# Performance work log

Measured on AMD Instinct MI355X. Metric: run time of the kernel, lower is better.

Reference implementation:

```python
import math
import jax, jax.numpy as jnp
import numpy as np

EPS = 1e-5
NUM_HEADS = 8

def gelu(x):
    return jax.nn.gelu(x, approximate=False)  # keras 'gelu' is exact

def layernorm(x, g, b):
    m = jnp.mean(x, axis=-1, keepdims=True)
    v = jnp.var(x, axis=-1, keepdims=True)
    return (x - m) * jax.lax.rsqrt(v + EPS) * g + b

def setup_inputs() -> dict:
    key = jax.random.key(0)
    ks = jax.random.split(key, 12)
    B, S, N, D = 2, 1, 2048, 256
    E = 256  # dim_emb == dim_out
    s_in = 1.0 / np.sqrt(D).astype(np.float32)
    s_e = 1.0 / np.sqrt(E).astype(np.float32)
    s_h = 1.0 / np.sqrt(4 * E).astype(np.float32)
    return {
        "X": jax.random.normal(ks[0], (B, S, N, D), jnp.float32),
        "Wq": jax.random.normal(ks[1], (D, E), jnp.float32) * s_in,
        "Wk": jax.random.normal(ks[2], (D, E), jnp.float32) * s_in,
        "Wv": jax.random.normal(ks[3], (D, E), jnp.float32) * s_in,
        "Wm": jax.random.normal(ks[4], (E, E), jnp.float32) * s_e,
        "bm": jnp.zeros((E,), jnp.float32),
        "W1": jax.random.normal(ks[5], (E, 4 * E), jnp.float32) * s_e,
        "bf1": jnp.zeros((4 * E,), jnp.float32),
        "W2": jax.random.normal(ks[6], (4 * E, E), jnp.float32) * s_h,
        "bf2": jnp.zeros((E,), jnp.float32),
        "ln0_g": jnp.ones((D,), jnp.float32),
        "ln0_b": jnp.zeros((D,), jnp.float32),
        "ln1_g": jnp.ones((E,), jnp.float32),
        "ln1_b": jnp.zeros((E,), jnp.float32),
    }

def reference(X, Wq, Wk, Wv, Wm, bm, W1, bf1, W2, bf2, ln0_g, ln0_b, ln1_g, ln1_b):
    B, S, N, D = X.shape  # S == 1 (set-transformer singleton axis)
    E = Wq.shape[1]
    H = NUM_HEADS
    dh = E // H
    dim_KV = D  # softmax scale uses dim_KV, not head dim (faithful to source)

    # pre-layer-norm applies only to the Q branch; K/V use raw X
    Xn = layernorm(X, ln0_g, ln0_b)
    Q = Xn @ Wq                      # (B,1,N,E)
    K = X @ Wk
    V = X @ Wv
    X_res = Q                        # fc_res is None -> residual is Q

    def to_heads(T):                 # (B,1,N,E) -> (B,H,N,dh), split along last dim
        return T[:, 0].reshape(B, N, H, dh).transpose(0, 2, 1, 3)

    q, k, v = to_heads(Q), to_heads(K), to_heads(V)
    A = jnp.einsum('bhnd,bhmd->bhnm', q, k) * (1.0 / math.sqrt(dim_KV))  # (B,H,N,N)
    P = jax.nn.softmax(A, axis=-1)
    mh = jnp.einsum('bhnm,bhmd->bhnd', P, v)            # (B,H,N,dh)
    mh = mh.transpose(0, 2, 1, 3).reshape(B, 1, N, E)   # concat heads on last dim

    Hm = gelu(mh @ Wm + bm)          # fc_mix_heads has gelu activation
    H_after_res = Hm + X_res
    H_rff = layernorm(H_after_res, ln1_g, ln1_b)

    # rff: Dense(4E, gelu) then an extra explicit gelu, then Dense(E, gelu)
    h1 = gelu(gelu(H_rff @ W1 + bf1))
    h2 = gelu(h1 @ W2 + bf2)
    return H_after_res + h2
```

## Files before the change

kernel.cpp:

```cpp
#include <hip/hip_runtime.h>
#include <math.h>

#define NTOK 2048
#define EDIM 256
#define ROWS 4096
#define SLOT (ROWS * EDIM)

typedef __attribute__((ext_vector_type(8))) short bf16x8;
typedef __attribute__((ext_vector_type(4))) short bf16x4_t;
typedef __attribute__((ext_vector_type(4))) unsigned short u16x4;
typedef __attribute__((ext_vector_type(4))) float f32x4;
typedef __attribute__((ext_vector_type(4))) unsigned u32x4;
typedef __attribute__((ext_vector_type(2))) unsigned u32x2;

__device__ __forceinline__ float gelu_f(float x) {
    return 0.5f * x * (1.0f + erff(x * 0.70710678118654752f));
}
__device__ __forceinline__ unsigned short f2bf(float x) {
    unsigned u = __builtin_bit_cast(unsigned, x);
    u += 0x7FFFu + ((u >> 16) & 1u);
    return (unsigned short)(u >> 16);
}
__device__ __forceinline__ float bf2f(unsigned short h) {
    unsigned u = ((unsigned)h) << 16;
    return __builtin_bit_cast(float, u);
}
__device__ __forceinline__ unsigned pack2(float lo, float hi) {
    unsigned r;
    asm("v_cvt_pk_bf16_f32 %0, %1, %2" : "=v"(r) : "v"(lo), "v"(hi));
    return r;
}

__global__ __launch_bounds__(256) void trans_w(const float* __restrict__ Wq, const float* __restrict__ Wk,
                                               const float* __restrict__ Wv, const float* __restrict__ Wm,
                                               const float* __restrict__ W1, const float* __restrict__ W2,
                                               unsigned short* WqT, unsigned short* WkvT,
                                               unsigned short* WmT, unsigned short* W1T,
                                               unsigned short* W2T) {
    __shared__ float Ls[64][65];
    const int bid = blockIdx.x;
    const float* src;
    unsigned short* dst;
    int K, N, t;
    if (bid < 16)       { src = Wq; dst = WqT;             K = 256;  N = 256;  t = bid; }
    else if (bid < 32)  { src = Wk; dst = WkvT;            K = 256;  N = 256;  t = bid - 16; }
    else if (bid < 48)  { src = Wv; dst = WkvT + 256*256;  K = 256;  N = 256;  t = bid - 32; }
    else if (bid < 64)  { src = Wm; dst = WmT;             K = 256;  N = 256;  t = bid - 48; }
    else if (bid < 128) { src = W1; dst = W1T;             K = 256;  N = 1024; t = bid - 64; }
    else                { src = W2; dst = W2T;             K = 1024; N = 256;  t = bid - 128; }
    const int tn = N >> 6;
    const int k0 = (t / tn) * 64, n0 = (t % tn) * 64;
    const int r = threadIdx.x >> 2, cq = threadIdx.x & 3;
#pragma unroll
    for (int u = 0; u < 4; ++u) {
        const float4 v = *(const float4*)&src[(size_t)(k0 + r) * N + n0 + cq * 16 + u * 4];
        Ls[r][cq * 16 + u * 4 + 0] = v.x;
        Ls[r][cq * 16 + u * 4 + 1] = v.y;
        Ls[r][cq * 16 + u * 4 + 2] = v.z;
        Ls[r][cq * 16 + u * 4 + 3] = v.w;
    }
    __syncthreads();
#pragma unroll
    for (int hh = 0; hh < 2; ++hh) {
        bf16x8 o;
#pragma unroll
        for (int j = 0; j < 8; ++j) o[j] = (short)f2bf(Ls[cq * 16 + hh * 8 + j][r]);
        *(bf16x8*)&dst[(size_t)(n0 + r) * K + k0 + cq * 16 + hh * 8] = o;
    }
}

template <bool RAW>
__global__ __launch_bounds__(256) void ln_bf16(const float* __restrict__ X, const float* __restrict__ g,
                                               const float* __restrict__ b, unsigned short* __restrict__ Y,
                                               unsigned short* __restrict__ Yraw) {
    const int wave = threadIdx.x >> 6, lane = threadIdx.x & 63;
    const int row = blockIdx.x * 4 + wave;
    const float4 v = *(const float4*)&X[(size_t)row * EDIM + lane * 4];
    float s = v.x + v.y + v.z + v.w;
    float s2 = v.x * v.x + v.y * v.y + v.z * v.z + v.w * v.w;
#pragma unroll
    for (int off = 1; off < 64; off <<= 1) {
        s += __shfl_xor(s, off);
        s2 += __shfl_xor(s2, off);
    }
    const float mean = s * (1.0f / 256.0f);
    const float var = s2 * (1.0f / 256.0f) - mean * mean;
    const float rstd = rsqrtf(var + 1e-5f);
    const float4 gg = *(const float4*)&g[lane * 4];
    const float4 bb = *(const float4*)&b[lane * 4];
    u16x4 o;
    o[0] = f2bf((v.x - mean) * rstd * gg.x + bb.x);
    o[1] = f2bf((v.y - mean) * rstd * gg.y + bb.y);
    o[2] = f2bf((v.z - mean) * rstd * gg.z + bb.z);
    o[3] = f2bf((v.w - mean) * rstd * gg.w + bb.w);
    *(u16x4*)&Y[(size_t)row * EDIM + lane * 4] = o;
    if (RAW) {
        u16x4 rw;
        rw[0] = f2bf(v.x); rw[1] = f2bf(v.y); rw[2] = f2bf(v.z); rw[3] = f2bf(v.w);
        *(u16x4*)&Yraw[(size_t)row * EDIM + lane * 4] = rw;
    }
}

template <int EPI>
__global__ __launch_bounds__(256) void gemm_bf16(const unsigned short* __restrict__ A,
                                                 const unsigned short* __restrict__ Bt,
                                                 const float* __restrict__ bias,
                                                 const float* __restrict__ res,
                                                 float* __restrict__ outF,
                                                 unsigned short* __restrict__ outB,
                                                 int M, int N, int K) {
    __shared__ unsigned short As[32][72];
    __shared__ unsigned short Bs[64][72];
    const int tid = threadIdx.x;
    const int lane = tid & 63, wid = tid >> 6;
    const int c = lane & 15, g = lane >> 4;
    const int wm = wid & 1, wn = wid >> 1;
    const int row0 = blockIdx.y * 32, col0 = blockIdx.x * 64;
    const int sarow = tid >> 3, saq = tid & 7;
    const int sbrow = tid >> 2, sbq = tid & 3;
    f32x4 acc[2] = {};
    for (int k0 = 0; k0 < K; k0 += 64) {
        __syncthreads();
        {
            const bf16x8 a0 = *(const bf16x8*)&A[(size_t)(row0 + sarow) * K + k0 + saq * 8];
            const bf16x8* gb = (const bf16x8*)&Bt[(size_t)(col0 + sbrow) * K + k0 + sbq * 16];
            const bf16x8 b0 = gb[0], b1 = gb[1];
            *(bf16x8*)&As[sarow][saq * 8] = a0;
            *(bf16x8*)&Bs[sbrow][sbq * 16] = b0;
            *(bf16x8*)&Bs[sbrow][sbq * 16 + 8] = b1;
        }
        __syncthreads();
#pragma unroll
        for (int ks = 0; ks < 2; ++ks) {
            const bf16x8 af = *(const bf16x8*)&As[wm * 16 + c][ks * 32 + 8 * g];
#pragma unroll
            for (int ni = 0; ni < 2; ++ni) {
                const bf16x8 bv = *(const bf16x8*)&Bs[wn * 32 + ni * 16 + c][ks * 32 + 8 * g];
                acc[ni] = __builtin_amdgcn_mfma_f32_16x16x32_bf16(af, bv, acc[ni], 0, 0, 0);
            }
        }
    }
#pragma unroll
    for (int ni = 0; ni < 2; ++ni) {
        const int colx = col0 + wn * 32 + ni * 16 + c;
        const float bi = (EPI != 0) ? bias[colx] : 0.0f;
#pragma unroll
        for (int r = 0; r < 4; ++r) {
            const int rowx = row0 + wm * 16 + 4 * g + r;
            const size_t idx = (size_t)rowx * N + colx;
            float v = acc[ni][r];
            if (EPI == 1) v = res[idx] + gelu_f(v + bi);
            else if (EPI == 2) v = gelu_f(gelu_f(v + bi));
            if (outF) outF[idx] = v;
            if (outB) outB[idx] = f2bf(v);
        }
    }
}

__global__ __launch_bounds__(256) void attn_mfma(const unsigned short* __restrict__ Qb,
                                                 const unsigned short* __restrict__ KVb,
                                                 float* __restrict__ Opart,
                                                 float* __restrict__ ML) {
    __shared__ unsigned short Ks[2][64][40];
    __shared__ unsigned short Vt[2][32][68];
    __shared__ float Otf[4][16][36];
    const int tid = threadIdx.x, lane = tid & 63, wid = tid >> 6;
    const int c = lane & 15, g = lane >> 4;
    const int bid = blockIdx.x;
    const int qt = bid & 31, h = (bid >> 5) & 7, b = (bid >> 8) & 1, s = bid >> 9;
    const int qrow = b * NTOK + qt * 64 + wid * 16;
    const int skey = tid >> 2, skq = tid & 3;
    const int vkp = tid & 31, vdq = tid >> 5;
    const size_t kvbase = (size_t)b * NTOK * 512 + h * 32;
    const int key0 = s * 1024;

    bf16x8 qf;
    {
        const bf16x8 qraw = *(const bf16x8*)&Qb[(size_t)(qrow + c) * EDIM + h * 32 + 8 * g];
#pragma unroll
        for (int j = 0; j < 8; ++j)
            qf[j] = (short)f2bf(bf2f((unsigned short)qraw[j]) * 0.09016844f);
    }
    const f32x4 zero4 = {0.0f, 0.0f, 0.0f, 0.0f};
    f32x4 accO[2] = {zero4, zero4};
    float lsum = 0.0f;

    {
        const int c0 = key0;
        const bf16x8 kr = *(const bf16x8*)&KVb[kvbase + (size_t)(c0 + skey) * 512 + skq * 8];
        const u16x4 v0 = *(const u16x4*)&KVb[kvbase + (size_t)(c0 + 2 * vkp) * 512 + 256 + vdq * 4];
        const u16x4 v1 = *(const u16x4*)&KVb[kvbase + (size_t)(c0 + 2 * vkp + 1) * 512 + 256 + vdq * 4];
        *(bf16x8*)&Ks[0][skey][skq * 8] = kr;
#pragma unroll
        for (int i = 0; i < 4; ++i)
            *(unsigned*)&Vt[0][vdq * 4 + i][2 * vkp] = ((unsigned)v1[i] << 16) | (unsigned)v0[i];
    }
    __syncthreads();

    for (int t = 0; t < 16; ++t) {
        const int cur = t & 1;
        bf16x8 kr2;
        u32x4 vr2;
        if (t < 15) {
            const int c0 = key0 + (t + 1) * 64;
            kr2 = *(const bf16x8*)&KVb[kvbase + (size_t)(c0 + skey) * 512 + skq * 8];
            const u16x4 v0 = *(const u16x4*)&KVb[kvbase + (size_t)(c0 + 2 * vkp) * 512 + 256 + vdq * 4];
            const u16x4 v1 = *(const u16x4*)&KVb[kvbase + (size_t)(c0 + 2 * vkp + 1) * 512 + 256 + vdq * 4];
#pragma unroll
            for (int i = 0; i < 4; ++i) vr2[i] = ((unsigned)v1[i] << 16) | (unsigned)v0[i];
        }

        f32x4 st[4];
#pragma unroll
        for (int t4 = 0; t4 < 4; ++t4) {
            const bf16x8 kf = *(const bf16x8*)&Ks[cur][t4 * 16 + c][8 * g];
            st[t4] = __builtin_amdgcn_mfma_f32_16x16x32_bf16(kf, qf, zero4, 0, 0, 0);
        }
#pragma unroll
        for (int t4 = 0; t4 < 4; ++t4)
#pragma unroll
            for (int r = 0; r < 4; ++r) {
                const float e = exp2f(st[t4][r]);
                st[t4][r] = e;
                lsum += e;
            }

        unsigned pk[8];
#pragma unroll
        for (int t4 = 0; t4 < 4; ++t4)
#pragma unroll
            for (int b2 = 0; b2 < 2; ++b2)
                pk[2 * t4 + b2] = pack2(st[t4][2 * b2], st[t4][2 * b2 + 1]);

        const int ghi = g >> 1;
        const int glo = g & 1;
#pragma unroll
        for (int kc = 0; kc < 2; ++kc) {
            u32x4 bw;
#pragma unroll
            for (int w = 0; w < 4; ++w) {
                const unsigned lo = pk[4 * kc + (w & 1)];
                const unsigned hi = pk[4 * kc + 2 + (w & 1)];
                const unsigned val = ghi ? hi : lo;
                const int srcLane = (2 * glo + (w >> 1)) * 16 + c;
                bw[w] = (unsigned)__shfl((int)val, srcLane);
            }
            const bf16x8 bpv = __builtin_bit_cast(bf16x8, bw);
#pragma unroll
            for (int dt = 0; dt < 2; ++dt) {
                const bf16x4_t vlo = *(const bf16x4_t*)&Vt[cur][c + 16 * dt][8 * g + 32 * kc];
                const bf16x4_t vhi = *(const bf16x4_t*)&Vt[cur][c + 16 * dt][8 * g + 32 * kc + 4];
                const u32x2 L = __builtin_bit_cast(u32x2, vlo);
                const u32x2 H2 = __builtin_bit_cast(u32x2, vhi);
                const u32x4 q4 = {L[0], L[1], H2[0], H2[1]};
                const bf16x8 vf = __builtin_bit_cast(bf16x8, q4);
                accO[dt] = __builtin_amdgcn_mfma_f32_16x16x32_bf16(vf, bpv, accO[dt], 0, 0, 0);
            }
        }

        if (t < 15) {
            *(bf16x8*)&Ks[cur ^ 1][skey][skq * 8] = kr2;
#pragma unroll
            for (int i = 0; i < 4; ++i)
                *(unsigned*)&Vt[cur ^ 1][vdq * 4 + i][2 * vkp] = vr2[i];
            __syncthreads();
        }
    }

    lsum += __shfl_xor(lsum, 16);
    lsum += __shfl_xor(lsum, 32);
    const float inv = 1.0f / lsum;
#pragma unroll
    for (int dt = 0; dt < 2; ++dt)
#pragma unroll
        for (int r = 0; r < 4; ++r)
            Otf[wid][c][dt * 16 + 4 * g + r] = accO[dt][r] * inv;
    if (g == 0) {
        *(float2*)&ML[(((size_t)s * 4096 + qrow + c) * 8 + h) * 2] = make_float2(0.0f, lsum);
    }
    const int oq = lane >> 2, odq = lane & 3;
    float* op = Opart + (size_t)s * SLOT + (size_t)(qrow + oq) * EDIM + h * 32 + odq * 8;
    const f32x4 o0 = *(const f32x4*)&Otf[wid][oq][odq * 8];
    const f32x4 o1 = *(const f32x4*)&Otf[wid][oq][odq * 8 + 4];
    *(f32x4*)&op[0] = o0;
    *(f32x4*)&op[4] = o1;
}

__global__ __launch_bounds__(256) void attn_combine(const float* __restrict__ Opart,
                                                    const float* __restrict__ ML,
                                                    unsigned short* __restrict__ mhb) {
    const int flat4 = blockIdx.x * 256 + threadIdx.x;
    const int row = flat4 >> 6;
    const int col = (flat4 & 63) * 4;
    const int h = col >> 5;
    const float2 ml0 = *(const float2*)&ML[(((size_t)0 * 4096 + row) * 8 + h) * 2];
    const float2 ml1 = *(const float2*)&ML[(((size_t)1 * 4096 + row) * 8 + h) * 2];
    const float M = fmaxf(ml0.x, ml1.x);
    const float a0 = ml0.y * exp2f(ml0.x - M);
    const float a1 = ml1.y * exp2f(ml1.x - M);
    const float inv = 1.0f / (a0 + a1);
    const f32x4 o0 = *(const f32x4*)&Opart[(size_t)row * EDIM + col];
    const f32x4 o1 = *(const f32x4*)&Opart[(size_t)SLOT + (size_t)row * EDIM + col];
    u16x4 r;
#pragma unroll
    for (int j = 0; j < 4; ++j) r[j] = f2bf((a0 * o0[j] + a1 * o1[j]) * inv);
    *(u16x4*)&mhb[(size_t)row * EDIM + col] = r;
}

extern "C" void kernel_launch(void* const* d_in, const int* in_sizes, int n_in,
                              void* d_out, int out_size, void* d_ws, size_t ws_size,
                              hipStream_t stream) {
    const float* X    = (const float*)d_in[0];
    const float* Wq   = (const float*)d_in[1];
    const float* Wk   = (const float*)d_in[2];
    const float* Wv   = (const float*)d_in[3];
    const float* Wm   = (const float*)d_in[4];
    const float* bm   = (const float*)d_in[5];
    const float* W1   = (const float*)d_in[6];
    const float* bf1  = (const float*)d_in[7];
    const float* W2   = (const float*)d_in[8];
    const float* bf2  = (const float*)d_in[9];
    const float* ln0g = (const float*)d_in[10];
    const float* ln0b = (const float*)d_in[11];
    const float* ln1g = (const float*)d_in[12];
    const float* ln1b = (const float*)d_in[13];
    float* out = (float*)d_out;
    char* w = (char*)d_ws;

    unsigned short* WqT  = (unsigned short*)(w + 0);
    unsigned short* WkvT = (unsigned short*)(w + 131072);
    unsigned short* WmT  = (unsigned short*)(w + 393216);
    unsigned short* W1T  = (unsigned short*)(w + 524288);
    unsigned short* W2T  = (unsigned short*)(w + 1048576);
    unsigned short* Xb   = (unsigned short*)(w + 1572864);
    float*          ML   = (float*)(w + 1572864);
    unsigned short* Xnb  = (unsigned short*)(w + 3670016);
    unsigned short* Qb   = (unsigned short*)(w + 5767168);
    float*          Qf   = (float*)(w + 7864320);
    unsigned short* KVb  = (unsigned short*)(w + 12058624);
    unsigned short* mhb  = (unsigned short*)(w + 16252928);
    float*          Hres = (float*)(w + 18350080);
    unsigned short* Hrff = (unsigned short*)(w + 22544384);
    unsigned short* h1b  = (unsigned short*)(w + 24641536);
    float*          Opart= (float*)(w + 24641536);

    trans_w<<<192, 256, 0, stream>>>(Wq, Wk, Wv, Wm, W1, W2, WqT, WkvT, WmT, W1T, W2T);
    ln_bf16<true><<<ROWS / 4, 256, 0, stream>>>(X, ln0g, ln0b, Xnb, Xb);
    gemm_bf16<0><<<dim3(4, 128), 256, 0, stream>>>(Xnb, WqT, nullptr, nullptr, Qf, Qb, ROWS, 256, 256);
    gemm_bf16<0><<<dim3(8, 128), 256, 0, stream>>>(Xb, WkvT, nullptr, nullptr, nullptr, KVb, ROWS, 512, 256);
    attn_mfma<<<1024, 256, 0, stream>>>(Qb, KVb, Opart, ML);
    attn_combine<<<1024, 256, 0, stream>>>(Opart, ML, mhb);
    gemm_bf16<1><<<dim3(4, 128), 256, 0, stream>>>(mhb, WmT, bm, Qf, Hres, nullptr, ROWS, 256, 256);
    ln_bf16<false><<<ROWS / 4, 256, 0, stream>>>(Hres, ln1g, ln1b, Hrff, nullptr);
    gemm_bf16<2><<<dim3(16, 128), 256, 0, stream>>>(Hrff, W1T, bf1, nullptr, nullptr, h1b, ROWS, 1024, 256);
    gemm_bf16<1><<<dim3(4, 128), 256, 0, stream>>>(h1b, W2T, bf2, Hres, out, nullptr, ROWS, 256, 1024);
}
```

Baseline: 95.14 us.

## Split attention keys four ways, store bf16 partials, narrow GEMM tiles

Attention now splits the key range into four chunks instead of two, giving 2048 blocks with half the loop trips each. The per-split outputs are written as bf16 with only the row sum stored, and the combine kernel merges four partials. Shared memory for the output staging is aliased onto the K/V buffers, which needs an extra barrier. The GEMM gains a BN template so the N=256 GEMMs use 32-wide column tiles and launch twice as many blocks, aiming to fill more CUs. In exchange there is more combine traffic, extra bf16 rounding of the partial outputs, and less operand reuse per block.

```diff
diff --git a/kernel.cpp b/kernel.cpp
--- a/kernel.cpp
+++ b/kernel.cpp
@@ -101,7 +101,7 @@
     }
 }
 
-template <int EPI>
+template <int EPI, int BN>
 __global__ __launch_bounds__(256) void gemm_bf16(const unsigned short* __restrict__ A,
                                                  const unsigned short* __restrict__ Bt,
                                                  const float* __restrict__ bias,
@@ -109,40 +109,46 @@
                                                  float* __restrict__ outF,
                                                  unsigned short* __restrict__ outB,
                                                  int M, int N, int K) {
+    constexpr int NI = BN / 32;
     __shared__ unsigned short As[32][72];
-    __shared__ unsigned short Bs[64][72];
+    __shared__ unsigned short Bs[BN][72];
     const int tid = threadIdx.x;
     const int lane = tid & 63, wid = tid >> 6;
     const int c = lane & 15, g = lane >> 4;
     const int wm = wid & 1, wn = wid >> 1;
-    const int row0 = blockIdx.y * 32, col0 = blockIdx.x * 64;
+    const int row0 = blockIdx.y * 32, col0 = blockIdx.x * BN;
     const int sarow = tid >> 3, saq = tid & 7;
-    const int sbrow = tid >> 2, sbq = tid & 3;
-    f32x4 acc[2] = {};
+    f32x4 acc[NI] = {};
     for (int k0 = 0; k0 < K; k0 += 64) {
         __syncthreads();
         {
             const bf16x8 a0 = *(const bf16x8*)&A[(size_t)(row0 + sarow) * K + k0 + saq * 8];
-            const bf16x8* gb = (const bf16x8*)&Bt[(size_t)(col0 + sbrow) * K + k0 + sbq * 16];
-            const bf16x8 b0 = gb[0], b1 = gb[1];
             *(bf16x8*)&As[sarow][saq * 8] = a0;
-            *(bf16x8*)&Bs[sbrow][sbq * 16] = b0;
-            *(bf16x8*)&Bs[sbrow][sbq * 16 + 8] = b1;
+            if (BN == 64) {
+                const int sbrow = tid >> 2, sbq = tid & 3;
+                const bf16x8* gb = (const bf16x8*)&Bt[(size_t)(col0 + sbrow) * K + k0 + sbq * 16];
+                const bf16x8 b0 = gb[0], b1 = gb[1];
+                *(bf16x8*)&Bs[sbrow][sbq * 16] = b0;
+                *(bf16x8*)&Bs[sbrow][sbq * 16 + 8] = b1;
+            } else {
+                const bf16x8 b0 = *(const bf16x8*)&Bt[(size_t)(col0 + sarow) * K + k0 + saq * 8];
+                *(bf16x8*)&Bs[sarow][saq * 8] = b0;
+            }
         }
         __syncthreads();
 #pragma unroll
         for (int ks = 0; ks < 2; ++ks) {
             const bf16x8 af = *(const bf16x8*)&As[wm * 16 + c][ks * 32 + 8 * g];
 #pragma unroll
-            for (int ni = 0; ni < 2; ++ni) {
-                const bf16x8 bv = *(const bf16x8*)&Bs[wn * 32 + ni * 16 + c][ks * 32 + 8 * g];
+            for (int ni = 0; ni < NI; ++ni) {
+                const bf16x8 bv = *(const bf16x8*)&Bs[(wn * NI + ni) * 16 + c][ks * 32 + 8 * g];
                 acc[ni] = __builtin_amdgcn_mfma_f32_16x16x32_bf16(af, bv, acc[ni], 0, 0, 0);
             }
         }
     }
 #pragma unroll
-    for (int ni = 0; ni < 2; ++ni) {
-        const int colx = col0 + wn * 32 + ni * 16 + c;
+    for (int ni = 0; ni < NI; ++ni) {
+        const int colx = col0 + (wn * NI + ni) * 16 + c;
         const float bi = (EPI != 0) ? bias[colx] : 0.0f;
 #pragma unroll
         for (int r = 0; r < 4; ++r) {
@@ -159,11 +165,12 @@
 
 __global__ __launch_bounds__(256) void attn_mfma(const unsigned short* __restrict__ Qb,
                                                  const unsigned short* __restrict__ KVb,
-                                                 float* __restrict__ Opart,
+                                                 unsigned short* __restrict__ Opart,
                                                  float* __restrict__ ML) {
-    __shared__ unsigned short Ks[2][64][40];
-    __shared__ unsigned short Vt[2][32][68];
-    __shared__ float Otf[4][16][36];
+    __shared__ char smem[18944];
+    unsigned short (*Ks)[64][40] = (unsigned short (*)[64][40])smem;
+    unsigned short (*Vt)[32][68] = (unsigned short (*)[32][68])(smem + 10240);
+    float (*Otf)[16][36]         = (float (*)[16][36])smem;
     const int tid = threadIdx.x, lane = tid & 63, wid = tid >> 6;
     const int c = lane & 15, g = lane >> 4;
     const int bid = blockIdx.x;
@@ -172,7 +179,7 @@
     const int skey = tid >> 2, skq = tid & 3;
     const int vkp = tid & 31, vdq = tid >> 5;
     const size_t kvbase = (size_t)b * NTOK * 512 + h * 32;
-    const int key0 = s * 1024;
+    const int key0 = s * 512;
 
     bf16x8 qf;
     {
@@ -197,11 +204,11 @@
     }
     __syncthreads();
 
-    for (int t = 0; t < 16; ++t) {
+    for (int t = 0; t < 8; ++t) {
         const int cur = t & 1;
         bf16x8 kr2;
         u32x4 vr2;
-        if (t < 15) {
+        if (t < 7) {
             const int c0 = key0 + (t + 1) * 64;
             kr2 = *(const bf16x8*)&KVb[kvbase + (size_t)(c0 + skey) * 512 + skq * 8];
             const u16x4 v0 = *(const u16x4*)&KVb[kvbase + (size_t)(c0 + 2 * vkp) * 512 + 256 + vdq * 4];
@@ -258,7 +265,7 @@
             }
         }
 
-        if (t < 15) {
+        if (t < 7) {
             *(bf16x8*)&Ks[cur ^ 1][skey][skq * 8] = kr2;
 #pragma unroll
             for (int i = 0; i < 4; ++i)
@@ -269,6 +276,7 @@
 
     lsum += __shfl_xor(lsum, 16);
     lsum += __shfl_xor(lsum, 32);
+    __syncthreads();
     const float inv = 1.0f / lsum;
 #pragma unroll
     for (int dt = 0; dt < 2; ++dt)
@@ -276,34 +284,43 @@
         for (int r = 0; r < 4; ++r)
             Otf[wid][c][dt * 16 + 4 * g + r] = accO[dt][r] * inv;
     if (g == 0) {
-        *(float2*)&ML[(((size_t)s * 4096 + qrow + c) * 8 + h) * 2] = make_float2(0.0f, lsum);
+        ML[((size_t)s * 4096 + qrow + c) * 8 + h] = lsum;
     }
     const int oq = lane >> 2, odq = lane & 3;
-    float* op = Opart + (size_t)s * SLOT + (size_t)(qrow + oq) * EDIM + h * 32 + odq * 8;
-    const f32x4 o0 = *(const f32x4*)&Otf[wid][oq][odq * 8];
-    const f32x4 o1 = *(const f32x4*)&Otf[wid][oq][odq * 8 + 4];
-    *(f32x4*)&op[0] = o0;
-    *(f32x4*)&op[4] = o1;
-}
-
-__global__ __launch_bounds__(256) void attn_combine(const float* __restrict__ Opart,
+    const float* srcp = &Otf[wid][oq][odq * 8];
+    u32x4 packed;
+    packed[0] = pack2(srcp[0], srcp[1]);
+    packed[1] = pack2(srcp[2], srcp[3]);
+    packed[2] = pack2(srcp[4], srcp[5]);
+    packed[3] = pack2(srcp[6], srcp[7]);
+    *(u32x4*)&Opart[(size_t)s * SLOT + (size_t)(qrow + oq) * EDIM + h * 32 + odq * 8] = packed;
+}
+
+__global__ __launch_bounds__(256) void attn_combine(const unsigned short* __restrict__ Opart,
                                                     const float* __restrict__ ML,
                                                     unsigned short* __restrict__ mhb) {
     const int flat4 = blockIdx.x * 256 + threadIdx.x;
     const int row = flat4 >> 6;
     const int col = (flat4 & 63) * 4;
     const int h = col >> 5;
-    const float2 ml0 = *(const float2*)&ML[(((size_t)0 * 4096 + row) * 8 + h) * 2];
-    const float2 ml1 = *(const float2*)&ML[(((size_t)1 * 4096 + row) * 8 + h) * 2];
-    const float M = fmaxf(ml0.x, ml1.x);
-    const float a0 = ml0.y * exp2f(ml0.x - M);
-    const float a1 = ml1.y * exp2f(ml1.x - M);
-    const float inv = 1.0f / (a0 + a1);
-    const f32x4 o0 = *(const f32x4*)&Opart[(size_t)row * EDIM + col];
-    const f32x4 o1 = *(const f32x4*)&Opart[(size_t)SLOT + (size_t)row * EDIM + col];
+    float lw[4];
+    float lt = 0.0f;
+#pragma unroll
+    for (int s = 0; s < 4; ++s) {
+        lw[s] = ML[((size_t)s * 4096 + row) * 8 + h];
+        lt += lw[s];
+    }
+    const float inv = 1.0f / lt;
+    float a[4] = {0.0f, 0.0f, 0.0f, 0.0f};
+#pragma unroll
+    for (int s = 0; s < 4; ++s) {
+        const u16x4 p = *(const u16x4*)&Opart[(size_t)s * SLOT + (size_t)row * EDIM + col];
+#pragma unroll
+        for (int j = 0; j < 4; ++j) a[j] += lw[s] * bf2f((unsigned short)p[j]);
+    }
     u16x4 r;
 #pragma unroll
-    for (int j = 0; j < 4; ++j) r[j] = f2bf((a0 * o0[j] + a1 * o1[j]) * inv);
+    for (int j = 0; j < 4; ++j) r[j] = f2bf(a[j] * inv);
     *(u16x4*)&mhb[(size_t)row * EDIM + col] = r;
 }
 
@@ -342,16 +359,16 @@
     float*          Hres = (float*)(w + 18350080);
     unsigned short* Hrff = (unsigned short*)(w + 22544384);
     unsigned short* h1b  = (unsigned short*)(w + 24641536);
-    float*          Opart= (float*)(w + 24641536);
+    unsigned short* Opart= (unsigned short*)(w + 24641536);
 
     trans_w<<<192, 256, 0, stream>>>(Wq, Wk, Wv, Wm, W1, W2, WqT, WkvT, WmT, W1T, W2T);
     ln_bf16<true><<<ROWS / 4, 256, 0, stream>>>(X, ln0g, ln0b, Xnb, Xb);
-    gemm_bf16<0><<<dim3(4, 128), 256, 0, stream>>>(Xnb, WqT, nullptr, nullptr, Qf, Qb, ROWS, 256, 256);
-    gemm_bf16<0><<<dim3(8, 128), 256, 0, stream>>>(Xb, WkvT, nullptr, nullptr, nullptr, KVb, ROWS, 512, 256);
-    attn_mfma<<<1024, 256, 0, stream>>>(Qb, KVb, Opart, ML);
+    gemm_bf16<0, 32><<<dim3(8, 128), 256, 0, stream>>>(Xnb, WqT, nullptr, nullptr, Qf, Qb, ROWS, 256, 256);
+    gemm_bf16<0, 64><<<dim3(8, 128), 256, 0, stream>>>(Xb, WkvT, nullptr, nullptr, nullptr, KVb, ROWS, 512, 256);
+    attn_mfma<<<2048, 256, 0, stream>>>(Qb, KVb, Opart, ML);
     attn_combine<<<1024, 256, 0, stream>>>(Opart, ML, mhb);
-    gemm_bf16<1><<<dim3(4, 128), 256, 0, stream>>>(mhb, WmT, bm, Qf, Hres, nullptr, ROWS, 256, 256);
+    gemm_bf16<1, 32><<<dim3(8, 128), 256, 0, stream>>>(mhb, WmT, bm, Qf, Hres, nullptr, ROWS, 256, 256);
     ln_bf16<false><<<ROWS / 4, 256, 0, stream>>>(Hres, ln1g, ln1b, Hrff, nullptr);
-    gemm_bf16<2><<<dim3(16, 128), 256, 0, stream>>>(Hrff, W1T, bf1, nullptr, nullptr, h1b, ROWS, 1024, 256);
-    gemm_bf16<1><<<dim3(4, 128), 256, 0, stream>>>(h1b, W2T, bf2, Hres, out, nullptr, ROWS, 256, 1024);
-}
+    gemm_bf16<2, 64><<<dim3(16, 128), 256, 0, stream>>>(Hrff, W1T, bf1, nullptr, nullptr, h1b, ROWS, 1024, 256);
+    gemm_bf16<1, 32><<<dim3(8, 128), 256, 0, stream>>>(h1b, W2T, bf2, Hres, out, nullptr, ROWS, 256, 1024);
+}
```

Result: faster. 91.76 us (-3.6%).
